# Kernel optimization log

Hardware: AMD Instinct MI355X
Metric: run time of the kernel (lower is better)

## Reference

```python
import jax, jax.numpy as jnp
import numpy as np

HEADS1, HID, LSTM_H, OUT = 4, 64, 32, 2
NEG_SLOPE = 0.2
EPS = 1e-16


def gat_layer(x, src, dst, W, att_src, att_dst, bias, heads, out_ch):
    """PyG GATConv (concat=True, add_self_loops handled by caller)."""
    N = x.shape[0]
    h = (x @ W).reshape(N, heads, out_ch)                 # [N, H, C]
    a_s = jnp.sum(h * att_src, axis=-1)                    # [N, H]
    a_d = jnp.sum(h * att_dst, axis=-1)                    # [N, H]
    e = jax.nn.leaky_relu(a_s[src] + a_d[dst], NEG_SLOPE)  # [E, H]
    m = jax.ops.segment_max(e, dst, num_segments=N)        # scatter-softmax (stable)
    e = jnp.exp(e - jax.lax.stop_gradient(m)[dst])
    denom = jax.ops.segment_sum(e, dst, num_segments=N)
    alpha = e / (denom[dst] + EPS)                         # [E, H]
    msg = h[src] * alpha[..., None]                        # [E, H, C]
    out = jax.ops.segment_sum(msg, dst, num_segments=N)    # [N, H, C]
    return out.reshape(N, heads * out_ch) + bias


def lstm_last(seq, W_ih, W_hh, b_ih, b_hh, hidden):
    """Single-layer batch_first LSTM; returns last-step hidden state. Gate order i,f,g,o (torch)."""
    B = seq.shape[0]
    xT = jnp.transpose(seq, (1, 0, 2))  # [T, B, F]
    b = b_ih + b_hh

    def step(carry, xt):
        h, c = carry
        z = xt @ W_ih.T + h @ W_hh.T + b  # [B, 4H]
        i, f, g, o = jnp.split(z, 4, axis=-1)
        c = jax.nn.sigmoid(f) * c + jax.nn.sigmoid(i) * jnp.tanh(g)
        h = jax.nn.sigmoid(o) * jnp.tanh(c)
        return (h, c), None

    h0 = jnp.zeros((B, hidden), seq.dtype)
    (h, _), _ = jax.lax.scan(step, (h0, h0), xT)
    return h


def setup_inputs() -> dict:
    key = jax.random.key(0)
    ks = jax.random.split(key, 20)
    N, E, IN, T = 50000, 800000, 128, 50
    s = lambda k, shp: jax.random.normal(k, shp, jnp.float32) * 0.05
    inp = {
        "x": jax.random.normal(ks[0], (N, IN), jnp.float32),
        "edge_index": jax.random.randint(ks[1], (2, E), 0, N, jnp.int32),
        "sequences": jax.random.normal(ks[2], (N, T, 3), jnp.float32),
        # GATConv 1: in=128 -> 64 per head, 4 heads
        "W1": s(ks[3], (IN, HEADS1 * HID)),
        "att_src1": s(ks[4], (HEADS1, HID)),
        "att_dst1": s(ks[5], (HEADS1, HID)),
        "bias1": jnp.zeros((HEADS1 * HID,), jnp.float32),
        # GATConv 2: in=256 -> 64, 1 head
        "W2": s(ks[6], (HEADS1 * HID, HID)),
        "att_src2": s(ks[7], (1, HID)),
        "att_dst2": s(ks[8], (1, HID)),
        "bias2": jnp.zeros((HID,), jnp.float32),
        # LSTM(input_size=3, hidden_size=32)
        "W_ih": s(ks[9], (4 * LSTM_H, 3)),
        "W_hh": s(ks[10], (4 * LSTM_H, LSTM_H)),
        "b_ih": jnp.zeros((4 * LSTM_H,), jnp.float32),
        "b_hh": jnp.zeros((4 * LSTM_H,), jnp.float32),
        # fusion MLP: (64+32) -> 64 -> 2
        "Wf1": s(ks[11], (HID + LSTM_H, HID)),
        "bf1": jnp.zeros((HID,), jnp.float32),
        "Wf2": s(ks[12], (HID, OUT)),
        "bf2": jnp.zeros((OUT,), jnp.float32),
    }
    return inp


def reference(x, edge_index, sequences, W1, att_src1, att_dst1, bias1,
              W2, att_src2, att_dst2, bias2, W_ih, W_hh, b_ih, b_hh,
              Wf1, bf1, Wf2, bf2):
    N = x.shape[0]
    # PyG GATConv default add_self_loops=True
    loops = jnp.arange(N, dtype=edge_index.dtype)
    src = jnp.concatenate([edge_index[0], loops])
    dst = jnp.concatenate([edge_index[1], loops])

    g = jax.nn.elu(gat_layer(x, src, dst, W1, att_src1, att_dst1, bias1, HEADS1, HID))
    # dropout is identity in eval mode
    g = gat_layer(g, src, dst, W2, att_src2, att_dst2, bias2, 1, HID)  # [N, 64]

    t = lstm_last(sequences, W_ih, W_hh, b_ih, b_hh, LSTM_H)           # [N, 32]

    combined = jnp.concatenate([g, t], axis=1)
    h = jax.nn.relu(combined @ Wf1 + bf1)
    return h @ Wf2 + bf2
```

## Files before the change

kernel.cpp:

```cpp
#include <hip/hip_runtime.h>
#include <math.h>

#define HEADS1 4
#define HID 64
#define LSTM_H 32
#define IN_F 128
#define T_STEPS 50
#define NEG_SLOPE 0.2f
#define EPS_A 1e-16f

typedef __attribute__((ext_vector_type(8))) short short8;
typedef __attribute__((ext_vector_type(4))) float floatx4;
typedef __attribute__((ext_vector_type(4))) unsigned uint32x4;

__device__ __forceinline__ float frcp(float x) {
    float r;
    asm("v_rcp_f32 %0, %1" : "=v"(r) : "v"(x));
    return r;
}
__device__ __forceinline__ float sigf(float x) { return frcp(1.0f + __expf(-x)); }
__device__ __forceinline__ float tanhfast(float x) {
    float e = __expf(2.0f * x);
    return 1.0f - 2.0f * frcp(e + 1.0f);
}
__device__ __forceinline__ unsigned short f2bf(float f) {
    unsigned u = __float_as_uint(f);
    unsigned r = (u + 0x7FFFu + ((u >> 16) & 1u)) >> 16;
    return (unsigned short)r;
}
__device__ __forceinline__ float bf2f(unsigned short s) {
    return __uint_as_float(((unsigned)s) << 16);
}
__device__ __forceinline__ unsigned cvt_pk_bf16(float a, float b) {
    unsigned r;
    asm("v_cvt_pk_bf16_f32 %0, %1, %2" : "=v"(r) : "v"(a), "v"(b));
    return r;
}
__device__ __forceinline__ float lo16f(unsigned p) { return __uint_as_float(p << 16); }
__device__ __forceinline__ float hi16f(unsigned p) { return __uint_as_float(p & 0xffff0000u); }
__device__ __forceinline__ short8 bc8(uint32x4 v) { return __builtin_bit_cast(short8, v); }

template <int K, int NC>
__global__ __launch_bounds__(256) void gemm64(const float* __restrict__ A,
                                              const float* __restrict__ B,
                                              float* __restrict__ C, int M) {
    constexpr int KC = 32;
    __shared__ float As[KC][68];
    __shared__ float Bs[KC][64];
    const int row0 = blockIdx.x * 64;
    const int col0 = blockIdx.y * 64;
    const int tx = threadIdx.x & 15;
    const int ty = threadIdx.x >> 4;
    float acc[4][4] = {{0.f}};

    for (int k0 = 0; k0 < K; k0 += KC) {
        {
            const int kk = threadIdx.x & 31;
            const int rb = threadIdx.x >> 5;
#pragma unroll
            for (int r = 0; r < 8; r++) {
                int row = row0 + rb + r * 8;
                As[kk][rb + r * 8] = (row < M) ? A[(size_t)row * K + k0 + kk] : 0.0f;
            }
            const int c  = threadIdx.x & 63;
            const int kb = threadIdx.x >> 6;
#pragma unroll
            for (int q = 0; q < KC / 4; q++)
                Bs[kb + q * 4][c] = B[(size_t)(k0 + kb + q * 4) * NC + col0 + c];
        }
        __syncthreads();
#pragma unroll
        for (int kk = 0; kk < KC; kk++) {
            float4 a4 = *(const float4*)&As[kk][ty * 4];
            float4 b4 = *(const float4*)&Bs[kk][tx * 4];
            float av[4] = {a4.x, a4.y, a4.z, a4.w};
            float bv[4] = {b4.x, b4.y, b4.z, b4.w};
#pragma unroll
            for (int i = 0; i < 4; i++)
#pragma unroll
                for (int j = 0; j < 4; j++) acc[i][j] += av[i] * bv[j];
        }
        __syncthreads();
    }
#pragma unroll
    for (int i = 0; i < 4; i++) {
        int row = row0 + ty * 4 + i;
        if (row < M) {
            float4 v = make_float4(acc[i][0], acc[i][1], acc[i][2], acc[i][3]);
            *(float4*)&C[(size_t)row * NC + col0 + tx * 4] = v;
        }
    }
}

__global__ void att_scores(const float* __restrict__ h, const float* __restrict__ att_s,
                           const float* __restrict__ att_d, float* __restrict__ as_,
                           float* __restrict__ ad_, int NH, int Hmask) {
    int i = blockIdx.x * blockDim.x + threadIdx.x;
    if (i >= NH) return;
    int hh = i & Hmask;
    const float* row = h + (size_t)i * HID;
    float s = 0.0f, d = 0.0f;
#pragma unroll 8
    for (int c = 0; c < HID; c++) {
        float v = row[c];
        s += v * att_s[hh * HID + c];
        d += v * att_d[hh * HID + c];
    }
    as_[i] = s;
    ad_[i] = d;
}

__global__ void count_deg(const int* __restrict__ dsts, int E, int ET, int* __restrict__ cnt) {
    int e = blockIdx.x * blockDim.x + threadIdx.x;
    if (e >= ET) return;
    int d = (e < E) ? dsts[e] : (e - E);
    atomicAdd(&cnt[d], 1);
}

__global__ void scan1(const int* __restrict__ cnt, int* __restrict__ rowp,
                      int* __restrict__ bsum, int N) {
    __shared__ int tmp[256];
    int i = blockIdx.x * 256 + threadIdx.x;
    int v = (i < N) ? cnt[i] : 0;
    tmp[threadIdx.x] = v;
    __syncthreads();
    for (int off = 1; off < 256; off <<= 1) {
        int t = (threadIdx.x >= (unsigned)off) ? tmp[threadIdx.x - off] : 0;
        __syncthreads();
        tmp[threadIdx.x] += t;
        __syncthreads();
    }
    if (i < N) rowp[i] = tmp[threadIdx.x] - v;
    if (threadIdx.x == 255) bsum[blockIdx.x] = tmp[255];
}

__global__ void scan2(int* __restrict__ bsum, int nb) {
    __shared__ int tmp[256];
    int v = (threadIdx.x < (unsigned)nb) ? bsum[threadIdx.x] : 0;
    tmp[threadIdx.x] = v;
    __syncthreads();
    for (int off = 1; off < 256; off <<= 1) {
        int t = (threadIdx.x >= (unsigned)off) ? tmp[threadIdx.x - off] : 0;
        __syncthreads();
        tmp[threadIdx.x] += t;
        __syncthreads();
    }
    if (threadIdx.x < (unsigned)nb) bsum[threadIdx.x] = tmp[threadIdx.x] - v;
}

__global__ void scan3(int* __restrict__ rowp, const int* __restrict__ bsum, int N, int ET) {
    int i = blockIdx.x * 256 + threadIdx.x;
    if (i < N) rowp[i] += bsum[blockIdx.x];
    if (i == 0) rowp[N] = ET;
}

__global__ void scatter_edges(const int* __restrict__ dsts, int E, int ET,
                              const int* __restrict__ rowp, int* __restrict__ cursor,
                              int* __restrict__ eid) {
    int e = blockIdx.x * blockDim.x + threadIdx.x;
    if (e >= ET) return;
    int d = (e < E) ? dsts[e] : (e - E);
    int pos = atomicAdd(&cursor[d], 1);
    eid[rowp[d] + pos] = e;
}

__global__ __launch_bounds__(256)
void gat_agg4_sp(const int* __restrict__ srcs, int E,
                 const int* __restrict__ rowp, const int* __restrict__ eid,
                 const float* __restrict__ as_, const float* __restrict__ ad_,
                 const float* __restrict__ hfeat, const float* __restrict__ bias,
                 float* __restrict__ g, int N) {
    __shared__ float s_alpha[4][64][4];
    const int wave = threadIdx.x >> 6;
    const int lane = threadIdx.x & 63;
    const int head = lane >> 4;
    const int dst = blockIdx.x * 4 + wave;
    if (dst >= N) return;
    const int start = rowp[dst], end = rowp[dst + 1];
    const float4 adv = ((const float4*)ad_)[dst];
    const float4* h4 = (const float4*)hfeat;

    float4 dsum = make_float4(0.f, 0.f, 0.f, 0.f);
    float4 acc  = make_float4(0.f, 0.f, 0.f, 0.f);

    for (int i0 = start; i0 < end; i0 += 64) {
        int cnt = min(64, end - i0);
        int i = i0 + lane;
        int s = 0;
        if (i < end) {
            int e = eid[i];
            s = (e < E) ? srcs[e] : (e - E);
            float4 a = ((const float4*)as_)[s];
            float tx, ex;
            tx = a.x + adv.x; tx = (tx > 0.f) ? tx : NEG_SLOPE * tx; ex = __expf(tx);
            dsum.x += ex; s_alpha[wave][lane][0] = ex;
            tx = a.y + adv.y; tx = (tx > 0.f) ? tx : NEG_SLOPE * tx; ex = __expf(tx);
            dsum.y += ex; s_alpha[wave][lane][1] = ex;
            tx = a.z + adv.z; tx = (tx > 0.f) ? tx : NEG_SLOPE * tx; ex = __expf(tx);
            dsum.z += ex; s_alpha[wave][lane][2] = ex;
            tx = a.w + adv.w; tx = (tx > 0.f) ? tx : NEG_SLOPE * tx; ex = __expf(tx);
            dsum.w += ex; s_alpha[wave][lane][3] = ex;
        }
        __builtin_amdgcn_wave_barrier();
#pragma unroll 4
        for (int k = 0; k < cnt; k++) {
            float a_k = s_alpha[wave][k][head];
            int   s_k = __shfl(s, k);
            float4 hv = h4[(size_t)s_k * 64 + lane];
            acc.x += a_k * hv.x; acc.y += a_k * hv.y;
            acc.z += a_k * hv.z; acc.w += a_k * hv.w;
        }
        __builtin_amdgcn_wave_barrier();
    }
#pragma unroll
    for (int mk = 32; mk >= 1; mk >>= 1) {
        dsum.x += __shfl_xor(dsum.x, mk);
        dsum.y += __shfl_xor(dsum.y, mk);
        dsum.z += __shfl_xor(dsum.z, mk);
        dsum.w += __shfl_xor(dsum.w, mk);
    }
    float den = (head == 0) ? dsum.x : (head == 1) ? dsum.y : (head == 2) ? dsum.z : dsum.w;
    float inv = 1.0f / (den + EPS_A);
    float4 b4 = ((const float4*)bias)[lane];
    float4 r;
    r.x = acc.x * inv + b4.x; r.x = (r.x > 0.f) ? r.x : __expf(r.x) - 1.f;
    r.y = acc.y * inv + b4.y; r.y = (r.y > 0.f) ? r.y : __expf(r.y) - 1.f;
    r.z = acc.z * inv + b4.z; r.z = (r.z > 0.f) ? r.z : __expf(r.z) - 1.f;
    r.w = acc.w * inv + b4.w; r.w = (r.w > 0.f) ? r.w : __expf(r.w) - 1.f;
    ((float4*)g)[(size_t)dst * 64 + lane] = r;
}

__global__ __launch_bounds__(256)
void gat_agg1_sp(const int* __restrict__ srcs, int E,
                 const int* __restrict__ rowp, const int* __restrict__ eid,
                 const float* __restrict__ as_, const float* __restrict__ ad_,
                 const float* __restrict__ hfeat, const float* __restrict__ bias,
                 float* __restrict__ g, int N) {
    __shared__ float s_alpha[4][64];
    const int wave = threadIdx.x >> 6;
    const int lane = threadIdx.x & 63;
    const int dst = blockIdx.x * 4 + wave;
    if (dst >= N) return;
    const int start = rowp[dst], end = rowp[dst + 1];
    const float adv = ad_[dst];

    float dsum = 0.0f, acc = 0.0f;
    for (int i0 = start; i0 < end; i0 += 64) {
        int cnt = min(64, end - i0);
        int i = i0 + lane;
        int s = 0;
        if (i < end) {
            int e = eid[i];
            s = (e < E) ? srcs[e] : (e - E);
            float t = as_[s] + adv;
            t = (t > 0.f) ? t : NEG_SLOPE * t;
            float ex = __expf(t);
            dsum += ex;
            s_alpha[wave][lane] = ex;
        }
        __builtin_amdgcn_wave_barrier();
#pragma unroll 4
        for (int k = 0; k < cnt; k++) {
            float a_k = s_alpha[wave][k];
            int   s_k = __shfl(s, k);
            acc += a_k * hfeat[(size_t)s_k * 64 + lane];
        }
        __builtin_amdgcn_wave_barrier();
    }
#pragma unroll
    for (int mk = 32; mk >= 1; mk >>= 1) dsum += __shfl_xor(dsum, mk);
    g[(size_t)dst * 64 + lane] = acc / (dsum + EPS_A) + bias[lane];
}

__global__ void prep_wsplit(const float* __restrict__ Wih, const float* __restrict__ Whh,
                            const float* __restrict__ bih, const float* __restrict__ bhh,
                            uint32x4* __restrict__ wsp) {
    const int tid = threadIdx.x;
    const int kk = tid >> 7, sub = (tid >> 6) & 1, lane = tid & 63;
    const int grp = lane >> 4, col = lane & 15;
    const int krow = grp * 8;
    const int n = (sub + kk * 2) * 16 + col;
    float w[8];
    *(float4*)&w[0] = *(const float4*)&Whh[n * 32 + krow + 0];
    *(float4*)&w[4] = *(const float4*)&Whh[n * 32 + krow + 4];
    unsigned hi[8], lo[8];
#pragma unroll
    for (int j = 0; j < 8; j++) {
        unsigned short hs = f2bf(w[j]);
        hi[j] = hs;
        lo[j] = f2bf(w[j] - bf2f(hs));
    }
    uint32x4 BH = {hi[0] | (hi[1] << 16), hi[2] | (hi[3] << 16),
                   hi[4] | (hi[5] << 16), hi[6] | (hi[7] << 16)};
    uint32x4 BL = {lo[0] | (lo[1] << 16), lo[2] | (lo[3] << 16),
                   lo[4] | (lo[5] << 16), lo[6] | (lo[7] << 16)};
    float wi0 = Wih[n * 3 + 0], wi1 = Wih[n * 3 + 1], wi2 = Wih[n * 3 + 2];
    float bb = bih[n] + bhh[n];
    unsigned h0 = f2bf(wi0), h1 = f2bf(wi1), h2 = f2bf(wi2), hb = f2bf(bb);
    uint32x4 B2 = {0u, 0u, 0u, 0u};
    if (grp == 0) {
        unsigned bl_ = f2bf(bb - bf2f((unsigned short)hb));
        B2[0] = h0 | (h1 << 16); B2[1] = h2 | (hb << 16);
        B2[2] = h0 | (h1 << 16); B2[3] = h2 | (bl_ << 16);
    } else if (grp == 1) {
        unsigned l0 = f2bf(wi0 - bf2f((unsigned short)h0));
        unsigned l1 = f2bf(wi1 - bf2f((unsigned short)h1));
        unsigned l2 = f2bf(wi2 - bf2f((unsigned short)h2));
        B2[0] = l0 | (l1 << 16); B2[1] = l2;
    }
    wsp[((kk * 3 + 0) * 2 + sub) * 64 + lane] = B2;
    wsp[((kk * 3 + 1) * 2 + sub) * 64 + lane] = BH;
    wsp[((kk * 3 + 2) * 2 + sub) * 64 + lane] = BL;
}

__global__ __launch_bounds__(512)
__attribute__((amdgpu_waves_per_eu(2, 4)))
void lstm_mfma(const float* __restrict__ seq, const uint32x4* __restrict__ wsp,
               float* __restrict__ t_out, int N) {
    __shared__ float s_seq[9600];
    __shared__ float s_h[4][2][16][36];

    const int tid  = threadIdx.x;
    const int wave = tid >> 6, lane = tid & 63;
    const int pair = wave >> 1, sub = wave & 1;
    const int grp  = lane >> 4, col = lane & 15;
    const int node0 = blockIdx.x * 64 + pair * 16;

    {
        const size_t base  = (size_t)blockIdx.x * 9600;
        const size_t limit = (size_t)N * 150;
        for (int i = tid * 4; i < 9600; i += 512 * 4) {
            size_t g = base + i;
            float4 v;
            if (g + 3 < limit) {
                v = *(const float4*)&seq[g];
            } else {
                v.x = (g + 0 < limit) ? seq[g + 0] : 0.0f;
                v.y = (g + 1 < limit) ? seq[g + 1] : 0.0f;
                v.z = (g + 2 < limit) ? seq[g + 2] : 0.0f;
                v.w = (g + 3 < limit) ? seq[g + 3] : 0.0f;
            }
            *(float4*)&s_seq[i] = v;
        }
    }

#define LF(KK, W) wsp[(((KK) * 3 + (W)) * 2 + sub) * 64 + lane]
    uint32x4 B2_0 = LF(0, 0), BH_0 = LF(0, 1), BL_0 = LF(0, 2);
    uint32x4 B2_1 = LF(1, 0), BH_1 = LF(1, 1), BL_1 = LF(1, 2);
    uint32x4 B2_2 = LF(2, 0), BH_2 = LF(2, 1), BL_2 = LF(2, 2);
    uint32x4 B2_3 = LF(3, 0), BH_3 = LF(3, 1), BL_3 = LF(3, 2);
#undef LF
    asm volatile("" : "+v"(B2_0), "+v"(BH_0), "+v"(BL_0),
                      "+v"(B2_1), "+v"(BH_1), "+v"(BL_1),
                      "+v"(B2_2), "+v"(BH_2), "+v"(BL_2),
                      "+v"(B2_3), "+v"(BH_3), "+v"(BL_3));

    for (int i = tid; i < 4 * 2 * 16 * 36; i += 512) ((float*)s_h)[i] = 0.0f;
    __syncthreads();

    float cst0 = 0.f, cst1 = 0.f, cst2 = 0.f, cst3 = 0.f;
    float hn0 = 0.f, hn1 = 0.f, hn2 = 0.f, hn3 = 0.f;
    const floatx4 zac = {0.f, 0.f, 0.f, 0.f};

    const bool g0 = (grp == 0);
    const float* xrow = &s_seq[(pair * 16 + col) * 150];

#pragma unroll 1
    for (int t = 0; t < T_STEPS; t++) {
        float xv0 = xrow[t * 3 + 0];
        float xv1 = xrow[t * 3 + 1];
        float xv2 = xrow[t * 3 + 2];

        unsigned w0 = cvt_pk_bf16(xv0, xv1);
        unsigned w1 = cvt_pk_bf16(xv2, g0 ? 1.0f : 0.0f);
        float e0 = xv0 - lo16f(w0);
        float e1 = xv1 - hi16f(w0);
        float e2 = xv2 - lo16f(w1);
        unsigned w2 = g0 ? cvt_pk_bf16(e0, e1) : 0u;
        unsigned w3 = g0 ? cvt_pk_bf16(e2, 1.0f) : 0u;
        uint32x4 a2p = {w0, w1, w2, w3};
        short8 A2 = bc8(a2p);

        const float* hr = &s_h[pair][(t + 1) & 1][col][grp * 8];
        floatx4 h0 = *(const floatx4*)&hr[0];
        floatx4 h1 = *(const floatx4*)&hr[4];
        unsigned p0 = cvt_pk_bf16(h0[0], h0[1]);
        unsigned p1 = cvt_pk_bf16(h0[2], h0[3]);
        unsigned p2 = cvt_pk_bf16(h1[0], h1[1]);
        unsigned p3 = cvt_pk_bf16(h1[2], h1[3]);
        uint32x4 hip = {p0, p1, p2, p3};
        short8 Ahi = bc8(hip);
        unsigned q0 = cvt_pk_bf16(h0[0] - lo16f(p0), h0[1] - hi16f(p0));
        unsigned q1 = cvt_pk_bf16(h0[2] - lo16f(p1), h0[3] - hi16f(p1));
        unsigned q2 = cvt_pk_bf16(h1[0] - lo16f(p2), h1[1] - hi16f(p2));
        unsigned q3 = cvt_pk_bf16(h1[2] - lo16f(p3), h1[3] - hi16f(p3));
        uint32x4 lop = {q0, q1, q2, q3};
        short8 Alo = bc8(lop);

        floatx4 d0 = __builtin_amdgcn_mfma_f32_16x16x32_bf16(A2, bc8(B2_0), zac, 0, 0, 0);
        d0 = __builtin_amdgcn_mfma_f32_16x16x32_bf16(Alo, bc8(BH_0), d0, 0, 0, 0);
        d0 = __builtin_amdgcn_mfma_f32_16x16x32_bf16(Ahi, bc8(BL_0), d0, 0, 0, 0);
        d0 = __builtin_amdgcn_mfma_f32_16x16x32_bf16(Ahi, bc8(BH_0), d0, 0, 0, 0);
        floatx4 d1 = __builtin_amdgcn_mfma_f32_16x16x32_bf16(A2, bc8(B2_1), zac, 0, 0, 0);
        d1 = __builtin_amdgcn_mfma_f32_16x16x32_bf16(Alo, bc8(BH_1), d1, 0, 0, 0);
        d1 = __builtin_amdgcn_mfma_f32_16x16x32_bf16(Ahi, bc8(BL_1), d1, 0, 0, 0);
        d1 = __builtin_amdgcn_mfma_f32_16x16x32_bf16(Ahi, bc8(BH_1), d1, 0, 0, 0);
        floatx4 d2 = __builtin_amdgcn_mfma_f32_16x16x32_bf16(A2, bc8(B2_2), zac, 0, 0, 0);
        d2 = __builtin_amdgcn_mfma_f32_16x16x32_bf16(Alo, bc8(BH_2), d2, 0, 0, 0);
        d2 = __builtin_amdgcn_mfma_f32_16x16x32_bf16(Ahi, bc8(BL_2), d2, 0, 0, 0);
        d2 = __builtin_amdgcn_mfma_f32_16x16x32_bf16(Ahi, bc8(BH_2), d2, 0, 0, 0);
        floatx4 d3 = __builtin_amdgcn_mfma_f32_16x16x32_bf16(A2, bc8(B2_3), zac, 0, 0, 0);
        d3 = __builtin_amdgcn_mfma_f32_16x16x32_bf16(Alo, bc8(BH_3), d3, 0, 0, 0);
        d3 = __builtin_amdgcn_mfma_f32_16x16x32_bf16(Ahi, bc8(BL_3), d3, 0, 0, 0);
        d3 = __builtin_amdgcn_mfma_f32_16x16x32_bf16(Ahi, bc8(BH_3), d3, 0, 0, 0);

        {
            float ig, fg, gv, og;
            ig = sigf(d0[0]); fg = sigf(d1[0]); gv = tanhfast(d2[0]); og = sigf(d3[0]);
            cst0 = fg * cst0 + ig * gv; hn0 = og * tanhfast(cst0);
            ig = sigf(d0[1]); fg = sigf(d1[1]); gv = tanhfast(d2[1]); og = sigf(d3[1]);
            cst1 = fg * cst1 + ig * gv; hn1 = og * tanhfast(cst1);
            ig = sigf(d0[2]); fg = sigf(d1[2]); gv = tanhfast(d2[2]); og = sigf(d3[2]);
            cst2 = fg * cst2 + ig * gv; hn2 = og * tanhfast(cst2);
            ig = sigf(d0[3]); fg = sigf(d1[3]); gv = tanhfast(d2[3]); og = sigf(d3[3]);
            cst3 = fg * cst3 + ig * gv; hn3 = og * tanhfast(cst3);
        }

        float* hw = &s_h[pair][t & 1][4 * grp][sub * 16 + col];
        hw[0 * 36] = hn0; hw[1 * 36] = hn1; hw[2 * 36] = hn2; hw[3 * 36] = hn3;
        __syncthreads();
    }

    {
        int node = node0 + 4 * grp;
        const int c = sub * 16 + col;
        if (node + 0 < N) t_out[(size_t)(node + 0) * LSTM_H + c] = hn0;
        if (node + 1 < N) t_out[(size_t)(node + 1) * LSTM_H + c] = hn1;
        if (node + 2 < N) t_out[(size_t)(node + 2) * LSTM_H + c] = hn2;
        if (node + 3 < N) t_out[(size_t)(node + 3) * LSTM_H + c] = hn3;
    }
}

__global__ void fusion_kernel(const float* __restrict__ g2, const float* __restrict__ tt,
                              const float* __restrict__ Wf1, const float* __restrict__ bf1,
                              const float* __restrict__ Wf2, const float* __restrict__ bf2,
                              float* __restrict__ out, int N) {
    __shared__ float sW[96 * 64];
    __shared__ float sb1[64];
    __shared__ float sW2[128];
    for (int i = threadIdx.x; i < 96 * 64; i += 256) sW[i] = Wf1[i];
    if (threadIdx.x < 64) sb1[threadIdx.x] = bf1[threadIdx.x];
    if (threadIdx.x < 128) sW2[threadIdx.x] = Wf2[threadIdx.x];
    __syncthreads();
    const int wave = threadIdx.x >> 6;
    const int lane = threadIdx.x & 63;
    for (int n = blockIdx.x * 4 + wave; n < N; n += gridDim.x * 4) {
        const float* gn = g2 + (size_t)n * 64;
        const float* tn = tt + (size_t)n * 32;
        float acc = sb1[lane];
#pragma unroll 8
        for (int k = 0; k < 64; k++) acc += gn[k] * sW[k * 64 + lane];
#pragma unroll 8
        for (int k = 0; k < 32; k++) acc += tn[k] * sW[(64 + k) * 64 + lane];
        acc = fmaxf(acc, 0.0f);
        float o0 = acc * sW2[lane * 2 + 0];
        float o1 = acc * sW2[lane * 2 + 1];
#pragma unroll
        for (int mk = 32; mk >= 1; mk >>= 1) {
            o0 += __shfl_xor(o0, mk);
            o1 += __shfl_xor(o1, mk);
        }
        if (lane == 0) {
            out[(size_t)n * 2 + 0] = o0 + bf2[0];
            out[(size_t)n * 2 + 1] = o1 + bf2[1];
        }
    }
}

extern "C" void kernel_launch(void* const* d_in, const int* in_sizes, int n_in,
                              void* d_out, int out_size, void* d_ws, size_t ws_size,
                              hipStream_t stream) {
    const float* x      = (const float*)d_in[0];
    const int*   eidx   = (const int*)d_in[1];
    const float* seq    = (const float*)d_in[2];
    const float* W1     = (const float*)d_in[3];
    const float* att_s1 = (const float*)d_in[4];
    const float* att_d1 = (const float*)d_in[5];
    const float* bias1  = (const float*)d_in[6];
    const float* W2     = (const float*)d_in[7];
    const float* att_s2 = (const float*)d_in[8];
    const float* att_d2 = (const float*)d_in[9];
    const float* bias2  = (const float*)d_in[10];
    const float* Wih    = (const float*)d_in[11];
    const float* Whh    = (const float*)d_in[12];
    const float* bih    = (const float*)d_in[13];
    const float* bhh    = (const float*)d_in[14];
    const float* Wf1    = (const float*)d_in[15];
    const float* bf1    = (const float*)d_in[16];
    const float* Wf2    = (const float*)d_in[17];
    const float* bf2    = (const float*)d_in[18];
    float* out = (float*)d_out;

    const int N  = in_sizes[0] / IN_F;
    const int E  = in_sizes[1] / 2;
    const int ET = E + N;
    const int* srcs = eidx;
    const int* dsts = eidx + E;

    float* fws = (float*)d_ws;
    size_t o = 0;
    float* h1  = fws + o; o += (size_t)N * 256;
    float* g1  = fws + o; o += (size_t)N * 256;
    float* as1 = fws + o; o += (size_t)N * 4;
    float* ad1 = fws + o; o += (size_t)N * 4;
    int* cnt    = (int*)(fws + o);
    int* rowp   = cnt + N;
    int* cursor = rowp + N + 1;
    int* eid    = cursor + N;
    int* bsum   = eid + ET;
    uintptr_t wp_ = (uintptr_t)(bsum + 512);
    wp_ = (wp_ + 15) & ~(uintptr_t)15;
    uint32x4* wsp = (uint32x4*)wp_;
    float* h2 = h1;
    float* g2 = h1 + (size_t)N * 64;
    float* tt = h1 + (size_t)N * 128;
    float* as2 = as1; float* ad2 = ad1;

    const int nTiles = (N + 255) / 256;
    dim3 blk(256);

    hipMemsetAsync(cnt, 0, (size_t)N * sizeof(int), stream);
    hipMemsetAsync(cursor, 0, (size_t)N * sizeof(int), stream);
    count_deg<<<(ET + 255) / 256, blk, 0, stream>>>(dsts, E, ET, cnt);
    scan1<<<nTiles, blk, 0, stream>>>(cnt, rowp, bsum, N);
    scan2<<<1, blk, 0, stream>>>(bsum, nTiles);
    scan3<<<(N + 256) / 256, blk, 0, stream>>>(rowp, bsum, N, ET);
    scatter_edges<<<(ET + 255) / 256, blk, 0, stream>>>(dsts, E, ET, rowp, cursor, eid);

    prep_wsplit<<<1, 512, 0, stream>>>(Wih, Whh, bih, bhh, wsp);

    gemm64<128, 256><<<dim3((N + 63) / 64, 4), blk, 0, stream>>>(x, W1, h1, N);
    att_scores<<<(N * 4 + 255) / 256, blk, 0, stream>>>(h1, att_s1, att_d1, as1, ad1, N * 4, 3);
    gat_agg4_sp<<<(N + 3) / 4, blk, 0, stream>>>(srcs, E, rowp, eid, as1, ad1, h1, bias1, g1, N);

    lstm_mfma<<<(N + 63) / 64, dim3(512), 0, stream>>>(seq, wsp, tt, N);

    gemm64<256, 64><<<dim3((N + 63) / 64, 1), blk, 0, stream>>>(g1, W2, h2, N);
    att_scores<<<(N + 255) / 256, blk, 0, stream>>>(h2, att_s2, att_d2, as2, ad2, N, 0);
    gat_agg1_sp<<<(N + 3) / 4, blk, 0, stream>>>(srcs, E, rowp, eid, as2, ad2, h2, bias2, g2, N);

    fusion_kernel<<<512, blk, 0, stream>>>(g2, tt, Wf1, bf1, Wf2, bf2, out, N);
}
```

Baseline: 770.0 us.

## Replace FP32 SIMT GEMMs with split-bf16 MFMA GEMMs for GAT projections

Swaps the scalar FP32 tiled GEMM for an MFMA kernel that emulates FP32 using a three-product split-bf16 scheme (hi*hi, hi*lo, lo*hi). The weights are pre-transposed and split into hi and lo bf16 parts by a small prep kernel, and the activations are split on the fly from shared memory. This targets the compute cost of the two dense projections on matrix cores, in exchange for extra prep launches, conversion instructions and slightly reduced precision compared with true FP32.

```diff
diff --git a/kernel.cpp b/kernel.cpp
--- a/kernel.cpp
+++ b/kernel.cpp
@@ -40,56 +40,99 @@
 __device__ __forceinline__ float hi16f(unsigned p) { return __uint_as_float(p & 0xffff0000u); }
 __device__ __forceinline__ short8 bc8(uint32x4 v) { return __builtin_bit_cast(short8, v); }
 
+template <int KK>
+__global__ void prep_wt(const float* __restrict__ W, unsigned short* __restrict__ th,
+                        unsigned short* __restrict__ tl, int total, int NC) {
+    int i = blockIdx.x * 256 + threadIdx.x;
+    if (i >= total) return;
+    int n = i / KK, k = i - n * KK;
+    float v = W[k * NC + n];
+    unsigned short h = f2bf(v);
+    th[i] = h;
+    tl[i] = f2bf(v - bf2f(h));
+}
+
 template <int K, int NC>
-__global__ __launch_bounds__(256) void gemm64(const float* __restrict__ A,
-                                              const float* __restrict__ B,
-                                              float* __restrict__ C, int M) {
-    constexpr int KC = 32;
-    __shared__ float As[KC][68];
-    __shared__ float Bs[KC][64];
-    const int row0 = blockIdx.x * 64;
+__global__ __launch_bounds__(256)
+void gemm_mfma(const float* __restrict__ A, const unsigned short* __restrict__ Bth,
+               const unsigned short* __restrict__ Btl, float* __restrict__ C, int M) {
+    __shared__ float sA[128][44];
+    __shared__ unsigned short sBh[64][40];
+    __shared__ unsigned short sBl[64][40];
+    const int tid = threadIdx.x;
+    const int wave = tid >> 6, lane = tid & 63;
+    const int wr = wave >> 1, wc = wave & 1;
+    const int row0 = blockIdx.x * 128;
     const int col0 = blockIdx.y * 64;
-    const int tx = threadIdx.x & 15;
-    const int ty = threadIdx.x >> 4;
-    float acc[4][4] = {{0.f}};
-
-    for (int k0 = 0; k0 < K; k0 += KC) {
+    const int l15 = lane & 15, l4 = lane >> 4;
+
+    floatx4 acc[4][2];
+#pragma unroll
+    for (int rb = 0; rb < 4; rb++)
+#pragma unroll
+        for (int cb = 0; cb < 2; cb++) acc[rb][cb] = (floatx4){0.f, 0.f, 0.f, 0.f};
+
+    for (int k0 = 0; k0 < K; k0 += 32) {
+        __syncthreads();
+#pragma unroll
+        for (int q = 0; q < 4; q++) {
+            int idx = q * 256 + tid;
+            int row = idx >> 3, seg = idx & 7;
+            int gr = row0 + row;
+            float4 v = (gr < M) ? *(const float4*)&A[(size_t)gr * K + k0 + seg * 4]
+                                : make_float4(0.f, 0.f, 0.f, 0.f);
+            *(float4*)&sA[row][seg * 4] = v;
+        }
         {
-            const int kk = threadIdx.x & 31;
-            const int rb = threadIdx.x >> 5;
-#pragma unroll
-            for (int r = 0; r < 8; r++) {
-                int row = row0 + rb + r * 8;
-                As[kk][rb + r * 8] = (row < M) ? A[(size_t)row * K + k0 + kk] : 0.0f;
+            int col = tid >> 2, seg = tid & 3;
+            size_t gb = (size_t)(col0 + col) * K + k0 + seg * 8;
+            *(short8*)&sBh[col][seg * 8] = *(const short8*)&Bth[gb];
+            *(short8*)&sBl[col][seg * 8] = *(const short8*)&Btl[gb];
+        }
+        __syncthreads();
+
+        short8 bh0 = *(const short8*)&sBh[wc * 32 + 0 + l15][l4 * 8];
+        short8 bl0 = *(const short8*)&sBl[wc * 32 + 0 + l15][l4 * 8];
+        short8 bh1 = *(const short8*)&sBh[wc * 32 + 16 + l15][l4 * 8];
+        short8 bl1 = *(const short8*)&sBl[wc * 32 + 16 + l15][l4 * 8];
+
+#pragma unroll
+        for (int rb = 0; rb < 4; rb++) {
+            int row = wr * 64 + rb * 16 + l15;
+            floatx4 a0 = *(const floatx4*)&sA[row][l4 * 8 + 0];
+            floatx4 a1 = *(const floatx4*)&sA[row][l4 * 8 + 4];
+            unsigned p0 = cvt_pk_bf16(a0[0], a0[1]);
+            unsigned p1 = cvt_pk_bf16(a0[2], a0[3]);
+            unsigned p2 = cvt_pk_bf16(a1[0], a1[1]);
+            unsigned p3 = cvt_pk_bf16(a1[2], a1[3]);
+            uint32x4 hp = {p0, p1, p2, p3};
+            short8 Ah = bc8(hp);
+            unsigned q0 = cvt_pk_bf16(a0[0] - lo16f(p0), a0[1] - hi16f(p0));
+            unsigned q1 = cvt_pk_bf16(a0[2] - lo16f(p1), a0[3] - hi16f(p1));
+            unsigned q2 = cvt_pk_bf16(a1[0] - lo16f(p2), a1[1] - hi16f(p2));
+            unsigned q3 = cvt_pk_bf16(a1[2] - lo16f(p3), a1[3] - hi16f(p3));
+            uint32x4 lp = {q0, q1, q2, q3};
+            short8 Al = bc8(lp);
+
+            acc[rb][0] = __builtin_amdgcn_mfma_f32_16x16x32_bf16(Ah, bh0, acc[rb][0], 0, 0, 0);
+            acc[rb][0] = __builtin_amdgcn_mfma_f32_16x16x32_bf16(Ah, bl0, acc[rb][0], 0, 0, 0);
+            acc[rb][0] = __builtin_amdgcn_mfma_f32_16x16x32_bf16(Al, bh0, acc[rb][0], 0, 0, 0);
+            acc[rb][1] = __builtin_amdgcn_mfma_f32_16x16x32_bf16(Ah, bh1, acc[rb][1], 0, 0, 0);
+            acc[rb][1] = __builtin_amdgcn_mfma_f32_16x16x32_bf16(Ah, bl1, acc[rb][1], 0, 0, 0);
+            acc[rb][1] = __builtin_amdgcn_mfma_f32_16x16x32_bf16(Al, bh1, acc[rb][1], 0, 0, 0);
+        }
+    }
+
+#pragma unroll
+    for (int rb = 0; rb < 4; rb++)
+#pragma unroll
+        for (int cb = 0; cb < 2; cb++)
+#pragma unroll
+            for (int q = 0; q < 4; q++) {
+                int row = row0 + wr * 64 + rb * 16 + l4 * 4 + q;
+                int col = col0 + wc * 32 + cb * 16 + l15;
+                if (row < M) C[(size_t)row * NC + col] = acc[rb][cb][q];
             }
-            const int c  = threadIdx.x & 63;
-            const int kb = threadIdx.x >> 6;
-#pragma unroll
-            for (int q = 0; q < KC / 4; q++)
-                Bs[kb + q * 4][c] = B[(size_t)(k0 + kb + q * 4) * NC + col0 + c];
-        }
-        __syncthreads();
-#pragma unroll
-        for (int kk = 0; kk < KC; kk++) {
-            float4 a4 = *(const float4*)&As[kk][ty * 4];
-            float4 b4 = *(const float4*)&Bs[kk][tx * 4];
-            float av[4] = {a4.x, a4.y, a4.z, a4.w};
-            float bv[4] = {b4.x, b4.y, b4.z, b4.w};
-#pragma unroll
-            for (int i = 0; i < 4; i++)
-#pragma unroll
-                for (int j = 0; j < 4; j++) acc[i][j] += av[i] * bv[j];
-        }
-        __syncthreads();
-    }
-#pragma unroll
-    for (int i = 0; i < 4; i++) {
-        int row = row0 + ty * 4 + i;
-        if (row < M) {
-            float4 v = make_float4(acc[i][0], acc[i][1], acc[i][2], acc[i][3]);
-            *(float4*)&C[(size_t)row * NC + col0 + tx * 4] = v;
-        }
-    }
 }
 
 __global__ void att_scores(const float* __restrict__ h, const float* __restrict__ att_s,
@@ -521,6 +564,10 @@
     uintptr_t wp_ = (uintptr_t)(bsum + 512);
     wp_ = (wp_ + 15) & ~(uintptr_t)15;
     uint32x4* wsp = (uint32x4*)wp_;
+    unsigned short* w1h = (unsigned short*)(wsp + 1536);
+    unsigned short* w1l = w1h + 32768;
+    unsigned short* w2h = w1l + 32768;
+    unsigned short* w2l = w2h + 16384;
     float* h2 = h1;
     float* g2 = h1 + (size_t)N * 64;
     float* tt = h1 + (size_t)N * 128;
@@ -538,14 +585,16 @@
     scatter_edges<<<(ET + 255) / 256, blk, 0, stream>>>(dsts, E, ET, rowp, cursor, eid);
 
     prep_wsplit<<<1, 512, 0, stream>>>(Wih, Whh, bih, bhh, wsp);
-
-    gemm64<128, 256><<<dim3((N + 63) / 64, 4), blk, 0, stream>>>(x, W1, h1, N);
+    prep_wt<128><<<(32768 + 255) / 256, blk, 0, stream>>>(W1, w1h, w1l, 32768, 256);
+    prep_wt<256><<<(16384 + 255) / 256, blk, 0, stream>>>(W2, w2h, w2l, 16384, 64);
+
+    gemm_mfma<128, 256><<<dim3((N + 127) / 128, 4), blk, 0, stream>>>(x, w1h, w1l, h1, N);
     att_scores<<<(N * 4 + 255) / 256, blk, 0, stream>>>(h1, att_s1, att_d1, as1, ad1, N * 4, 3);
     gat_agg4_sp<<<(N + 3) / 4, blk, 0, stream>>>(srcs, E, rowp, eid, as1, ad1, h1, bias1, g1, N);
 
     lstm_mfma<<<(N + 63) / 64, dim3(512), 0, stream>>>(seq, wsp, tt, N);
 
-    gemm64<256, 64><<<dim3((N + 63) / 64, 1), blk, 0, stream>>>(g1, W2, h2, N);
+    gemm_mfma<256, 64><<<dim3((N + 127) / 128, 1), blk, 0, stream>>>(g1, w2h, w2l, h2, N);
     att_scores<<<(N + 255) / 256, blk, 0, stream>>>(h2, att_s2, att_d2, as2, ad2, N, 0);
     gat_agg1_sp<<<(N + 3) / 4, blk, 0, stream>>>(srcs, E, rowp, eid, as2, ad2, h2, bias2, g2, N);
 
```

New measurement: 731.4 us. 5.0% less time.
